# Performance work log

Hardware: AMD Instinct MI355X
Metric: run time of the kernel (lower is better)

Reference implementation:

```python
import jax, jax.numpy as jnp
import numpy as np

C = 256
E = C // 2  # embed_dim = in_channels / 2


def setup_inputs() -> dict:
    key = jax.random.key(0)
    ks = jax.random.split(key, 9)
    B, H, W = 8, 64, 64
    x = jax.random.normal(ks[0], (B, C, H, W), dtype=jnp.float32)
    s_in = 1.0 / np.sqrt(C)
    s_e = 1.0 / np.sqrt(E)
    wq = jax.random.uniform(ks[1], (E, C), jnp.float32, -s_in, s_in)
    bq = jax.random.uniform(ks[2], (E,), jnp.float32, -s_in, s_in)
    wk = jax.random.uniform(ks[3], (E, C), jnp.float32, -s_in, s_in)
    bk = jax.random.uniform(ks[4], (E,), jnp.float32, -s_in, s_in)
    wv = jax.random.uniform(ks[5], (E, C), jnp.float32, -s_in, s_in)
    bv = jax.random.uniform(ks[6], (E,), jnp.float32, -s_in, s_in)
    wo = jax.random.uniform(ks[7], (C, E), jnp.float32, -s_e, s_e)
    bo = jax.random.uniform(ks[8], (C,), jnp.float32, -s_e, s_e)
    return {"x": x, "wq": wq, "bq": bq, "wk": wk, "bk": bk,
            "wv": wv, "bv": bv, "wo": wo, "bo": bo}


def reference(x, wq, bq, wk, bk, wv, bv, wo, bo):
    B, Cc, H, W = x.shape
    N = H * W
    # flatten spatial: [B, N, C]; 1x1 conv == per-pixel linear over channels
    xf = x.reshape(B, Cc, N).transpose(0, 2, 1)
    q = jnp.einsum('bnc,ec->bne', xf, wq) + bq   # [B, N, E]
    k = jnp.einsum('bnc,ec->bne', xf, wk) + bk   # [B, N, E]
    v = jnp.einsum('bnc,ec->bne', xf, wv) + bv   # [B, N, E]
    attn_score = jnp.einsum('bne,bme->bnm', q, k)  # [B, N, N]
    attn_prob = jax.nn.softmax(attn_score, axis=-1)
    feat = jnp.einsum('bnm,bme->bne', attn_prob, v)  # [B, N, E]
    out = jnp.einsum('bne,ce->bnc', feat, wo) + bo   # expansion 1x1 conv
    out = out.transpose(0, 2, 1).reshape(B, Cc, H, W)
    return out + x
```

## Files before the change

kernel.cpp:

```cpp
#include <hip/hip_runtime.h>
#include <hip/hip_bf16.h>


typedef __attribute__((ext_vector_type(8))) short s16x8;
typedef __attribute__((ext_vector_type(4))) short s16x4;
typedef __attribute__((ext_vector_type(4))) float f32x4;

#define B_ 8
#define C_ 256
#define E_ 128
#define N_ 4096
#define SLICES 4
#define SLICE_KV (N_ / SLICES)
#define NTILES (SLICE_KV / 64)
#define PST 76
#define LOG2E 1.44269504f
#define SHIFT2 21.6404256f

#define GLDS16(g, l) __builtin_amdgcn_global_load_lds( \
    (const __attribute__((address_space(1))) void*)(g), \
    (__attribute__((address_space(3))) void*)(l), 16, 0, 0)

static __device__ __forceinline__ unsigned short f2bf(float f) {
    union { float f; unsigned int u; } v; v.f = f;
    return (unsigned short)((v.u + 0x7FFFu + ((v.u >> 16) & 1u)) >> 16);
}
static __device__ __forceinline__ float bf2f(unsigned short h) {
    union { unsigned int u; float f; } v; v.u = ((unsigned int)h) << 16;
    return v.f;
}

__global__ __launch_bounds__(256) void convert_w(
    const float* __restrict__ wq, const float* __restrict__ wk,
    const float* __restrict__ wv, const float* __restrict__ wo,
    unsigned short* __restrict__ wqb, unsigned short* __restrict__ wkb,
    unsigned short* __restrict__ wvb, unsigned short* __restrict__ wob)
{
    const int i = blockIdx.x * 256 + threadIdx.x;
    wqb[i] = f2bf(wq[i]);
    wkb[i] = f2bf(wk[i]);
    wvb[i] = f2bf(wv[i]);
    wob[i] = f2bf(wo[i]);
}

__global__ __launch_bounds__(256, 2) void qkv_kernel(
    const float* __restrict__ x,
    const unsigned short* __restrict__ wqb, const float* __restrict__ bq,
    const unsigned short* __restrict__ wkb, const float* __restrict__ bk,
    const unsigned short* __restrict__ wvb, const float* __restrict__ bv,
    unsigned short* __restrict__ Q, unsigned short* __restrict__ K,
    unsigned short* __restrict__ Vt)
{
    __shared__ unsigned short xs[64 * 264];

    const int tid = threadIdx.x;
    const int b  = blockIdx.x >> 6;
    const int n0 = (blockIdx.x & 63) << 6;

    {
        const int n  = tid & 63;
        const int c0 = tid >> 6;
        const float* xp = x + ((size_t)(b * C_) << 12) + n0 + n;
        for (int it = 0; it < 64; ++it) {
            const int c = it * 4 + c0;
            xs[n * 264 + c] = f2bf(xp[(size_t)c << 12]);
        }
    }
    __syncthreads();

    const int w = tid >> 6, l = tid & 63, hi = l >> 4, lx = l & 15;

    for (int idx = w; idx < 24; idx += 4) {
        const int out = idx >> 3;
        const int et  = idx & 7;
        const int e0  = et << 4;
        const unsigned short* W = (out == 0) ? wqb : (out == 1) ? wkb : wvb;
        const float* bias = (out == 0) ? bq : (out == 1) ? bk : bv;
        const float scale = (out == 0) ? LOG2E : 1.0f;

        s16x8 af[8];
        const unsigned short* wp = W + (e0 + lx) * C_ + hi * 8;
#pragma unroll
        for (int ks = 0; ks < 8; ++ks) af[ks] = *(const s16x8*)(wp + ks * 32);

        float bi[4];
#pragma unroll
        for (int r = 0; r < 4; ++r) bi[r] = bias[e0 + hi * 4 + r];

#pragma unroll
        for (int nt = 0; nt < 4; ++nt) {
            f32x4 acc = {0.f, 0.f, 0.f, 0.f};
#pragma unroll
            for (int ks = 0; ks < 8; ++ks) {
                s16x8 xb = *(const s16x8*)&xs[(nt * 16 + lx) * 264 + ks * 32 + hi * 8];
                acc = __builtin_amdgcn_mfma_f32_16x16x32_bf16(af[ks], xb, acc, 0, 0, 0);
            }
            const int n = n0 + nt * 16 + lx;
            if (out < 2) {
                unsigned short* dst =
                    ((out == 0) ? Q : K) + ((size_t)(b * N_ + n) << 7) + e0 + hi * 4;
                s16x4 pk;
#pragma unroll
                for (int r = 0; r < 4; ++r) pk[r] = (short)f2bf((acc[r] + bi[r]) * scale);
                *(s16x4*)dst = pk;
            } else {
#pragma unroll
                for (int r = 0; r < 4; ++r)
                    Vt[((size_t)(b * E_ + e0 + hi * 4 + r) << 12) + n] =
                        f2bf(acc[r] + bi[r]);
            }
        }
    }
}

__global__ __launch_bounds__(256, 2) void attn_partial(
    const unsigned short* __restrict__ Q, const unsigned short* __restrict__ K,
    const unsigned short* __restrict__ Vt,
    unsigned short* __restrict__ featP, float* __restrict__ denomP)
{
    __shared__ unsigned short Kx[64 * 128];
    __shared__ unsigned short Vs[128 * 64];
    __shared__ unsigned short Ps[4][32 * PST];

    const int tid = threadIdx.x;
    const int b   = blockIdx.x & 7;
    const int idx = blockIdx.x >> 3;
    const int sl  = idx >> 5;
    const int qt  = idx & 31;
    const int w = tid >> 6, l = tid & 63, hi = l >> 4, lx = l & 15;
    const int q0 = qt * 128 + w * 32;

    s16x8 qA[2][4];
#pragma unroll
    for (int qf = 0; qf < 2; ++qf) {
        const unsigned short* qp =
            Q + ((size_t)(b * N_ + q0 + qf * 16 + lx) << 7) + hi * 8;
#pragma unroll
        for (int ks = 0; ks < 4; ++ks) qA[qf][ks] = *(const s16x8*)(qp + ks * 32);
    }

    f32x4 feat[2][8];
#pragma unroll
    for (int qf = 0; qf < 2; ++qf)
#pragma unroll
        for (int ef = 0; ef < 8; ++ef) feat[qf][ef] = (f32x4){0.f, 0.f, 0.f, 0.f};
    float dAcc[8];
#pragma unroll
    for (int i = 0; i < 8; ++i) dAcc[i] = 0.f;

    const unsigned short* Kg = K + ((size_t)(b * N_) << 7);
    const unsigned short* Vg = Vt + ((size_t)(b * E_) << 12);
    unsigned short* pw = &Ps[w][0];


    for (int it = 0; it < NTILES; ++it) {
        const int kv0 = sl * SLICE_KV + it * 64;
        __syncthreads();
#pragma unroll
        for (int i = 0; i < 4; ++i) {
            const int flat = tid + i * 256;
            const int row = flat >> 4, c16 = flat & 15;
            GLDS16(Kg + (size_t)(kv0 + row) * 128 + ((c16 ^ (row & 7)) << 3),
                   &Kx[(i * 256 + w * 64) << 3]);
        }
#pragma unroll
        for (int i = 0; i < 4; ++i) {
            const int flat = tid + i * 256;
            const int e = flat >> 3, c8 = flat & 7;
            GLDS16(Vg + (((size_t)e << 12) + kv0) + ((c8 ^ (e & 7)) << 3),
                   &Vs[(i * 256 + w * 64) << 3]);
        }
        __syncthreads();

#pragma unroll
        for (int kvf = 0; kvf < 4; ++kvf) {
            f32x4 s0 = {0.f, 0.f, 0.f, 0.f}, s1 = {0.f, 0.f, 0.f, 0.f};
#pragma unroll
            for (int ks = 0; ks < 4; ++ks) {
                s16x8 kb = *(const s16x8*)&Kx[((kvf * 16 + lx) << 7) +
                                              (((ks * 4 + hi) ^ (lx & 7)) << 3)];
                s0 = __builtin_amdgcn_mfma_f32_16x16x32_bf16(qA[0][ks], kb, s0, 0, 0, 0);
                s1 = __builtin_amdgcn_mfma_f32_16x16x32_bf16(qA[1][ks], kb, s1, 0, 0, 0);
            }
#pragma unroll
            for (int r = 0; r < 4; ++r) {
                float p0 = __builtin_exp2f(s0[r] - SHIFT2);
                float p1 = __builtin_exp2f(s1[r] - SHIFT2);
                dAcc[r]     += p0;
                dAcc[4 + r] += p1;
                pw[(hi * 4 + r) * PST      + kvf * 16 + lx] = f2bf(p0);
                pw[(16 + hi * 4 + r) * PST + kvf * 16 + lx] = f2bf(p1);
            }
        }
#pragma unroll
        for (int ks = 0; ks < 2; ++ks) {
            s16x8 pa0 = *(const s16x8*)&pw[(lx)      * PST + ks * 32 + hi * 8];
            s16x8 pa1 = *(const s16x8*)&pw[(16 + lx) * PST + ks * 32 + hi * 8];
#pragma unroll
            for (int ef = 0; ef < 8; ++ef) {
                s16x8 vb = *(const s16x8*)&Vs[((ef * 16 + lx) << 6) +
                                              (((ks * 4 + hi) ^ (lx & 7)) << 3)];
                feat[0][ef] = __builtin_amdgcn_mfma_f32_16x16x32_bf16(pa0, vb, feat[0][ef], 0, 0, 0);
                feat[1][ef] = __builtin_amdgcn_mfma_f32_16x16x32_bf16(pa1, vb, feat[1][ef], 0, 0, 0);
            }
        }
    }

#pragma unroll
    for (int i = 0; i < 8; ++i) {
        float v = dAcc[i];
        v += __shfl_xor(v, 1); v += __shfl_xor(v, 2);
        v += __shfl_xor(v, 4); v += __shfl_xor(v, 8);
        dAcc[i] = v;
    }
    const size_t qg = (size_t)((sl * 8 + b) * N_ + q0);
    if (lx == 0) {
        float* dP = denomP + qg;
#pragma unroll
        for (int qf = 0; qf < 2; ++qf)
#pragma unroll
            for (int r = 0; r < 4; ++r)
                dP[qf * 16 + hi * 4 + r] = dAcc[qf * 4 + r];
    }
    unsigned short* fP = featP + (qg << 7);
#pragma unroll
    for (int qf = 0; qf < 2; ++qf)
#pragma unroll
        for (int ef = 0; ef < 8; ++ef)
#pragma unroll
            for (int r = 0; r < 4; ++r)
                fP[(qf * 16 + hi * 4 + r) * 128 + ef * 16 + lx] =
                    f2bf(feat[qf][ef][r]);
}

__global__ __launch_bounds__(256, 2) void combine_kernel(
    const unsigned short* __restrict__ featP, const float* __restrict__ denomP,
    const unsigned short* __restrict__ wob, const float* __restrict__ bo,
    const float* __restrict__ x, float* __restrict__ out)
{
    __shared__ unsigned short fs[64 * 136];

    const int tid = threadIdx.x;
    const int b  = blockIdx.x & 7;
    const int nt = blockIdx.x >> 3;

    {
        const int q = tid >> 2, eb = (tid & 3) * 32;
        const int n = nt * 64 + q;
        float den = 0.f;
#pragma unroll
        for (int s = 0; s < SLICES; ++s)
            den += denomP[(size_t)((s * 8 + b) * N_) + n];
        const float inv = 1.f / den;
#pragma unroll
        for (int e8 = 0; e8 < 4; ++e8) {
            float acc[8];
#pragma unroll
            for (int j = 0; j < 8; ++j) acc[j] = 0.f;
#pragma unroll
            for (int s = 0; s < SLICES; ++s) {
                s16x8 v = *(const s16x8*)(featP +
                    (((size_t)((s * 8 + b) * N_) + n) << 7) + eb + e8 * 8);
#pragma unroll
                for (int j = 0; j < 8; ++j) acc[j] += bf2f((unsigned short)v[j]);
            }
            s16x8 o;
#pragma unroll
            for (int j = 0; j < 8; ++j) o[j] = (short)f2bf(acc[j] * inv);
            *(s16x8*)&fs[q * 136 + eb + e8 * 8] = o;
        }
    }
    __syncthreads();

    const int w = tid >> 6, l = tid & 63, hi = l >> 4, lx = l & 15;

    s16x8 fa[4];
#pragma unroll
    for (int ks = 0; ks < 4; ++ks)
        fa[ks] = *(const s16x8*)&fs[(w * 16 + lx) * 136 + ks * 32 + hi * 8];

    const int n = nt * 64 + w * 16 + lx;
    const float* xb = x + ((size_t)(b * C_) << 12);
    float* ob = out + ((size_t)(b * C_) << 12);
#pragma unroll 1
    for (int ct = 0; ct < 16; ++ct) {
        const unsigned short* wp = wob + (ct * 16 + lx) * 128 + hi * 8;
        f32x4 acc = {0.f, 0.f, 0.f, 0.f};
#pragma unroll
        for (int ks = 0; ks < 4; ++ks) {
            s16x8 wb = *(const s16x8*)(wp + ks * 32);
            acc = __builtin_amdgcn_mfma_f32_16x16x32_bf16(wb, fa[ks], acc, 0, 0, 0);
        }
#pragma unroll
        for (int r = 0; r < 4; ++r) {
            const int c = ct * 16 + hi * 4 + r;
            const size_t off = ((size_t)c << 12) + n;
            ob[off] = acc[r] + bo[c] + xb[off];
        }
    }
}

extern "C" void kernel_launch(void* const* d_in, const int* in_sizes, int n_in,
                              void* d_out, int out_size, void* d_ws, size_t ws_size,
                              hipStream_t stream) {
    (void)in_sizes; (void)n_in; (void)out_size; (void)ws_size;
    const float* x  = (const float*)d_in[0];
    const float* wq = (const float*)d_in[1];
    const float* bq = (const float*)d_in[2];
    const float* wk = (const float*)d_in[3];
    const float* bk = (const float*)d_in[4];
    const float* wv = (const float*)d_in[5];
    const float* bv = (const float*)d_in[6];
    const float* wo = (const float*)d_in[7];
    const float* bo = (const float*)d_in[8];

    unsigned short* Q  = (unsigned short*)d_ws;
    unsigned short* K  = Q + (size_t)B_ * N_ * E_;
    unsigned short* Vt = K + (size_t)B_ * N_ * E_;
    unsigned short* featP = Vt + (size_t)B_ * N_ * E_;
    float* denomP = (float*)(featP + (size_t)SLICES * B_ * N_ * E_);
    unsigned short* wqb = (unsigned short*)(denomP + (size_t)SLICES * B_ * N_);
    unsigned short* wkb = wqb + E_ * C_;
    unsigned short* wvb = wkb + E_ * C_;
    unsigned short* wob = wvb + E_ * C_;

    convert_w<<<dim3(128), dim3(256), 0, stream>>>(
        wq, wk, wv, wo, wqb, wkb, wvb, wob);
    qkv_kernel<<<dim3(B_ * (N_ / 64)), dim3(256), 0, stream>>>(
        x, wqb, bq, wkb, bk, wvb, bv, Q, K, Vt);
    attn_partial<<<dim3(B_ * 32 * SLICES), dim3(256), 0, stream>>>(
        Q, K, Vt, featP, denomP);
    combine_kernel<<<dim3(B_ * 64), dim3(256), 0, stream>>>(
        featP, denomP, wob, bo, x, (float*)d_out);
}
```

Measured before the change: 175.8 us.

## Halve KV slices, use padded register-staged LDS loads, hardware bf16 pack

Cuts the key/value split from four slices to two, so there are half as many attention blocks, each looping over twice as many tiles, and the combine pass reads fewer partial results. Replaces the direct global-to-LDS swizzled loads with ordinary vector loads through registers into padded LDS rows. Replaces the software bf16 rounding with the packed v_cvt_pk_bf16_f32 instruction. Fewer blocks lowers parallelism, and loading through registers can raise register pressure and adds LDS write latency.

```diff
diff --git a/kernel.cpp b/kernel.cpp
--- a/kernel.cpp
+++ b/kernel.cpp
@@ -10,17 +10,13 @@
 #define C_ 256
 #define E_ 128
 #define N_ 4096
-#define SLICES 4
+#define SLICES 2
 #define SLICE_KV (N_ / SLICES)
 #define NTILES (SLICE_KV / 64)
 #define PST 76
 #define LOG2E 1.44269504f
 #define SHIFT2 21.6404256f
 
-#define GLDS16(g, l) __builtin_amdgcn_global_load_lds( \
-    (const __attribute__((address_space(1))) void*)(g), \
-    (__attribute__((address_space(3))) void*)(l), 16, 0, 0)
-
 static __device__ __forceinline__ unsigned short f2bf(float f) {
     union { float f; unsigned int u; } v; v.f = f;
     return (unsigned short)((v.u + 0x7FFFu + ((v.u >> 16) & 1u)) >> 16);
@@ -28,6 +24,11 @@
 static __device__ __forceinline__ float bf2f(unsigned short h) {
     union { unsigned int u; float f; } v; v.u = ((unsigned int)h) << 16;
     return v.f;
+}
+static __device__ __forceinline__ unsigned int cvtbf2(float lo, float hi) {
+    unsigned int r;
+    asm("v_cvt_pk_bf16_f32 %0, %1, %2" : "=v"(r) : "v"(lo), "v"(hi));
+    return r;
 }
 
 __global__ __launch_bounds__(256) void convert_w(
@@ -118,8 +119,8 @@
     const unsigned short* __restrict__ Vt,
     unsigned short* __restrict__ featP, float* __restrict__ denomP)
 {
-    __shared__ unsigned short Kx[64 * 128];
-    __shared__ unsigned short Vs[128 * 64];
+    __shared__ unsigned short Ks[64 * 136];
+    __shared__ unsigned short Vs[128 * 72];
     __shared__ unsigned short Ps[4][32 * PST];
 
     const int tid = threadIdx.x;
@@ -152,7 +153,6 @@
     const unsigned short* Vg = Vt + ((size_t)(b * E_) << 12);
     unsigned short* pw = &Ps[w][0];
 
-
     for (int it = 0; it < NTILES; ++it) {
         const int kv0 = sl * SLICE_KV + it * 64;
         __syncthreads();
@@ -160,15 +160,15 @@
         for (int i = 0; i < 4; ++i) {
             const int flat = tid + i * 256;
             const int row = flat >> 4, c16 = flat & 15;
-            GLDS16(Kg + (size_t)(kv0 + row) * 128 + ((c16 ^ (row & 7)) << 3),
-                   &Kx[(i * 256 + w * 64) << 3]);
+            *(s16x8*)&Ks[row * 136 + c16 * 8] =
+                *(const s16x8*)(Kg + (size_t)(kv0 + row) * 128 + c16 * 8);
         }
 #pragma unroll
         for (int i = 0; i < 4; ++i) {
             const int flat = tid + i * 256;
-            const int e = flat >> 3, c8 = flat & 7;
-            GLDS16(Vg + (((size_t)e << 12) + kv0) + ((c8 ^ (e & 7)) << 3),
-                   &Vs[(i * 256 + w * 64) << 3]);
+            const int e = flat >> 3, c16 = flat & 7;
+            *(s16x8*)&Vs[e * 72 + c16 * 8] =
+                *(const s16x8*)(Vg + ((size_t)e << 12) + kv0 + c16 * 8);
         }
         __syncthreads();
 
@@ -177,8 +177,7 @@
             f32x4 s0 = {0.f, 0.f, 0.f, 0.f}, s1 = {0.f, 0.f, 0.f, 0.f};
 #pragma unroll
             for (int ks = 0; ks < 4; ++ks) {
-                s16x8 kb = *(const s16x8*)&Kx[((kvf * 16 + lx) << 7) +
-                                              (((ks * 4 + hi) ^ (lx & 7)) << 3)];
+                s16x8 kb = *(const s16x8*)&Ks[(kvf * 16 + lx) * 136 + ks * 32 + hi * 8];
                 s0 = __builtin_amdgcn_mfma_f32_16x16x32_bf16(qA[0][ks], kb, s0, 0, 0, 0);
                 s1 = __builtin_amdgcn_mfma_f32_16x16x32_bf16(qA[1][ks], kb, s1, 0, 0, 0);
             }
@@ -188,8 +187,9 @@
                 float p1 = __builtin_exp2f(s1[r] - SHIFT2);
                 dAcc[r]     += p0;
                 dAcc[4 + r] += p1;
-                pw[(hi * 4 + r) * PST      + kvf * 16 + lx] = f2bf(p0);
-                pw[(16 + hi * 4 + r) * PST + kvf * 16 + lx] = f2bf(p1);
+                const unsigned int pk = cvtbf2(p0, p1);
+                pw[(hi * 4 + r) * PST      + kvf * 16 + lx] = (unsigned short)pk;
+                pw[(16 + hi * 4 + r) * PST + kvf * 16 + lx] = (unsigned short)(pk >> 16);
             }
         }
 #pragma unroll
@@ -198,8 +198,7 @@
             s16x8 pa1 = *(const s16x8*)&pw[(16 + lx) * PST + ks * 32 + hi * 8];
 #pragma unroll
             for (int ef = 0; ef < 8; ++ef) {
-                s16x8 vb = *(const s16x8*)&Vs[((ef * 16 + lx) << 6) +
-                                              (((ks * 4 + hi) ^ (lx & 7)) << 3)];
+                s16x8 vb = *(const s16x8*)&Vs[(ef * 16 + lx) * 72 + ks * 32 + hi * 8];
                 feat[0][ef] = __builtin_amdgcn_mfma_f32_16x16x32_bf16(pa0, vb, feat[0][ef], 0, 0, 0);
                 feat[1][ef] = __builtin_amdgcn_mfma_f32_16x16x32_bf16(pa1, vb, feat[1][ef], 0, 0, 0);
             }
@@ -230,7 +229,7 @@
 #pragma unroll
             for (int r = 0; r < 4; ++r)
                 fP[(qf * 16 + hi * 4 + r) * 128 + ef * 16 + lx] =
-                    f2bf(feat[qf][ef][r]);
+                    (unsigned short)cvtbf2(feat[qf][ef][r], 0.f);
 }
 
 __global__ __launch_bounds__(256, 2) void combine_kernel(
@@ -266,7 +265,8 @@
             }
             s16x8 o;
 #pragma unroll
-            for (int j = 0; j < 8; ++j) o[j] = (short)f2bf(acc[j] * inv);
+            for (int j = 0; j < 8; ++j)
+                o[j] = (short)(unsigned short)cvtbf2(acc[j] * inv, 0.f);
             *(s16x8*)&fs[q * 136 + eb + e8 * 8] = o;
         }
     }
```

Result: no change. 174.4 us (-0.8%).
